# Optimization experiments

Hardware: AMD Instinct MI355X
Metric: run time of the kernel (lower is better)

The kernel has to match this reference:

```python
import jax, jax.numpy as jnp
import numpy as np

NUM_HEADS = 4
KEY_DIMS = 32  # c // num_heads


def rel_to_abs(x):
    # x: [B, N, W, 2W-1] relative logits -> [B, N, W, W] absolute logits
    b, n, w, _ = x.shape
    x = jnp.pad(x, ((0, 0), (0, 0), (0, 0), (0, 1)))           # [b,n,w,2w]
    x = x.reshape(b, n, w * 2 * w)
    x = jnp.pad(x, ((0, 0), (0, 0), (0, w - 1)))
    x = x.reshape(b, n, w + 1, 2 * w - 1)
    return x[:, :, :w, w - 1:]


def rel_logits_1d(q, rel_k):
    # q: [B, heads, X, Y, d], rel_k: [2Y-1, d] -> [B, heads, X, X, Y, Y]
    b, nh, xx, yy, d = q.shape
    rl = jnp.einsum('bhxyd,md->bhxym', q, rel_k)               # [b,h,x,y,2y-1]
    rl = rel_to_abs(rl.reshape(b, nh * xx, yy, 2 * yy - 1))    # [b,h*x,y,y]
    rl = rl.reshape(b, nh, xx, 1, yy, yy)
    return jnp.broadcast_to(rl, (b, nh, xx, xx, yy, yy))


def relative_position_bias(pos_q, pos_emb_h, pos_emb_w):
    # pos_q: [B, heads, H, W, d] -> bias [B, heads, H, W, H, W]
    rw = rel_logits_1d(pos_q, pos_emb_w)                        # [b,h,H,H,W,W]
    rw = rw.transpose(0, 1, 2, 4, 3, 5)                         # [b,h,H,W,H,W]
    rh = rel_logits_1d(pos_q.transpose(0, 1, 3, 2, 4), pos_emb_h)  # [b,h,W,W,H,H]
    rh = rh.transpose(0, 1, 4, 2, 5, 3)                         # [b,h,H,W,H,W]
    return rw + rh


def setup_inputs() -> dict:
    key = jax.random.key(0)
    k1, k2, k3, k4 = jax.random.split(key, 4)
    B, H, W, C = 2, 64, 64, 128
    qk_dims = NUM_HEADS * KEY_DIMS  # 128
    out_channels = C
    x = jax.random.normal(k1, (B, H, W, C), dtype=jnp.float32)
    w_qkv = jax.random.normal(k2, (C, 2 * qk_dims + out_channels), dtype=jnp.float32) * 0.05
    pos_emb_h = jax.random.normal(k3, (2 * H - 1, KEY_DIMS), dtype=jnp.float32) * 0.05
    pos_emb_w = jax.random.normal(k4, (2 * W - 1, KEY_DIMS), dtype=jnp.float32) * 0.05
    return {'x': x, 'w_qkv': w_qkv, 'pos_emb_h': pos_emb_h, 'pos_emb_w': pos_emb_w}


def reference(x, w_qkv, pos_emb_h, pos_emb_w):
    B, H, W, C = x.shape
    nh, kd = NUM_HEADS, KEY_DIMS
    qk_dims = nh * kd
    oc = C
    scale = 1.0 / float(kd) ** 0.5

    qkv = jnp.einsum('bhwc,cd->bhwd', x, w_qkv)                 # 1x1 conv, no bias
    q, k, v = jnp.split(qkv, [qk_dims, 2 * qk_dims], axis=-1)
    L = H * W
    q = q.reshape(B, L, nh, kd).transpose(0, 2, 1, 3)           # [B,nh,L,kd]
    k = k.reshape(B, L, nh, kd).transpose(0, 2, 1, 3)           # [B,nh,L,kd]
    v = v.reshape(B, L, nh, oc // nh).transpose(0, 2, 1, 3)     # [B,nh,L,dv]

    pos_q = q.reshape(B, nh, H, W, kd)
    pos = relative_position_bias(pos_q, pos_emb_h, pos_emb_w).reshape(B, nh, L, L)

    scores = jnp.einsum('bnqd,bnkd->bnqk', q, k) * scale + pos  # [B,nh,L,L]
    attn = jax.nn.softmax(scores, axis=-1)
    out = jnp.einsum('bnqk,bnkd->bnqd', attn, v)                # [B,nh,L,dv]
    out = out.transpose(0, 2, 1, 3).reshape(B, H, W, oc)
    return out
```

## Files before the change

### kernel.cpp

```cpp
#include <hip/hip_runtime.h>
#include <hip/hip_bf16.h>
#include <math.h>

#define B_  2
#define NH  4
#define HH  64
#define WW  64
#define KD  32
#define L_  4096
#define BN_ 8
#define LOG2E 1.4426950408889634f
#define KSCALE (0.17677669529663687f * 1.4426950408889634f)
#define FIXED_M 10.0f

typedef float    f32x4  __attribute__((ext_vector_type(4), may_alias));
typedef _Float16 half8  __attribute__((ext_vector_type(8), may_alias));
typedef _Float16 half4  __attribute__((ext_vector_type(4), may_alias));
typedef __fp16   fp16x2 __attribute__((ext_vector_type(2)));
typedef unsigned uint4v __attribute__((ext_vector_type(4)));

__device__ __forceinline__ float fexp2(float x) {
#if __has_builtin(__builtin_amdgcn_exp2f)
    return __builtin_amdgcn_exp2f(x);
#else
    return __expf(x * 0.69314718056f);
#endif
}

__device__ __forceinline__ unsigned pack2u(float a, float b) {
    fp16x2 t = __builtin_amdgcn_cvt_pkrtz(a, b);
    union { fp16x2 i; unsigned o; } u;
    u.i = t;
    return u.o;
}

__global__ __launch_bounds__(256) void qkv_gemm(const float* __restrict__ x,
                                                const float* __restrict__ w,
                                                _Float16* __restrict__ q_h,
                                                _Float16* __restrict__ k_h,
                                                _Float16* __restrict__ vt_h) {
    __shared__ __align__(16) char smem[34816];
    _Float16* xs  = (_Float16*)smem;
    _Float16* wsT = (_Float16*)(smem + 17408);

    const int mt = blockIdx.x % 128;
    const int nt = blockIdx.x / 128;
    const int m0 = mt * 64, n0 = nt * 64;
    const int tid = threadIdx.x;
    const int wv = tid >> 6, lane = tid & 63;
    const int l16 = lane & 15, quad = lane >> 4;

    #pragma unroll
    for (int i = 0; i < 8; i++) {
        const int idx = i * 256 + tid;
        const int row = idx >> 5, c4 = (idx & 31) * 4;
        const float4 v = *(const float4*)&x[(size_t)(m0 + row) * 128 + c4];
        half4 h;
        h[0] = (_Float16)v.x; h[1] = (_Float16)v.y;
        h[2] = (_Float16)v.z; h[3] = (_Float16)v.w;
        *(half4*)&xs[row * 136 + c4] = h;
    }
    #pragma unroll
    for (int i = 0; i < 8; i++) {
        const int idx = i * 256 + tid;
        const int k = idx >> 4, c4 = (idx & 15) * 4;
        const float4 v = *(const float4*)&w[(size_t)k * 384 + n0 + c4];
        wsT[(c4 + 0) * 136 + k] = (_Float16)v.x;
        wsT[(c4 + 1) * 136 + k] = (_Float16)v.y;
        wsT[(c4 + 2) * 136 + k] = (_Float16)v.z;
        wsT[(c4 + 3) * 136 + k] = (_Float16)v.w;
    }
    __syncthreads();

    f32x4 acc[4] = {{0.f,0.f,0.f,0.f},{0.f,0.f,0.f,0.f},
                    {0.f,0.f,0.f,0.f},{0.f,0.f,0.f,0.f}};
    half8 af[4];
    #pragma unroll
    for (int kc = 0; kc < 4; kc++)
        af[kc] = *(const half8*)&xs[(wv * 16 + l16) * 136 + kc * 32 + quad * 8];
    #pragma unroll
    for (int ns = 0; ns < 4; ns++)
        #pragma unroll
        for (int kc = 0; kc < 4; kc++) {
            const half8 bf = *(const half8*)&wsT[(ns * 16 + l16) * 136 + kc * 32 + quad * 8];
            acc[ns] = __builtin_amdgcn_mfma_f32_16x16x32_f16(af[kc], bf, acc[ns], 0, 0, 0);
        }

    const int which = n0 >> 7;
    const int nc = n0 & 127;
    const int b = m0 >> 12;
    if (which < 2) {
        _Float16* dst = (which == 0) ? q_h : k_h;
        const float mult = (which == 1) ? KSCALE : 1.0f;
        #pragma unroll
        for (int ns = 0; ns < 4; ns++) {
            const int col = nc + ns * 16 + l16;
            const int bn = b * NH + (col >> 5);
            const int d = col & 31;
            #pragma unroll
            for (int r = 0; r < 4; r++) {
                const int l = (m0 & 4095) + wv * 16 + quad * 4 + r;
                dst[((size_t)bn * L_ + l) * 32 + d] = (_Float16)(acc[ns][r] * mult);
            }
        }
    } else {
        __syncthreads();
        float* img = (float*)smem;
        #pragma unroll
        for (int ns = 0; ns < 4; ns++) {
            const int chan = ns * 16 + l16;
            const int h = chan >> 5, d = chan & 31;
            #pragma unroll
            for (int r = 0; r < 4; r++) {
                const int p = wv * 16 + quad * 4 + r;
                const int y = p >> 5, p32 = p & 31;
                const int q4 = (p32 >> 2) & 3;
                const int j = ((p32 >> 4) & 1) * 4 + (p32 & 3);
                const int fidx = h * 2048 + (y * 2 + (d >> 4)) * 512
                               + (q4 * 16 + (d & 15)) * 8 + j;
                img[fidx + (fidx >> 4)] = acc[ns][r];
            }
        }
        __syncthreads();
        const int ktg = (m0 & 4095) >> 6;
        #pragma unroll
        for (int h = 0; h < 2; h++) {
            const int head = (nc >> 5) + h;
            const int bn = b * NH + head;
            const int fbase = h * 2048 + tid * 8;
            const int sbase = fbase + (fbase >> 4);
            half8 o;
            #pragma unroll
            for (int e = 0; e < 8; e++) o[e] = (_Float16)img[sbase + e];
            *(half8*)(vt_h + (size_t)bn * 131072 + ktg * 2048 + tid * 8) = o;
        }
    }
}

__global__ __launch_bounds__(512, 4) void attn_mfma(
    const _Float16* __restrict__ q_h,
    const _Float16* __restrict__ k_h,
    const _Float16* __restrict__ vt_h,
    const float* __restrict__ emb_h,
    const float* __restrict__ emb_w,
    float* __restrict__ out)
{
    __shared__ __align__(16) char smem[33792];

    const int bi   = blockIdx.x;
    const int bn   = bi & 7;
    const int w1   = bi >> 3;
    const int tid  = threadIdx.x;
    const int wv   = tid >> 6;
    const int qwv  = wv & 3;
    const int kh   = wv >> 2;
    const int lane = tid & 63;
    const int l16  = lane & 15;
    const int quad = lane >> 4;
    const int q0   = qwv * 16;

    float* Rl = (float*)smem;

    const half8 aq = *(const half8*)(q_h +
        (((size_t)bn * L_ + (q0 + l16) * 64 + w1) * 32 + quad * 8));

    const _Float16* Kbase = k_h  + (size_t)bn * L_ * 32;
    const _Float16* Vtile = vt_h + (size_t)bn * 131072;
    const int lo = lane * 8;
    const int kt0 = kh * 32;
    const int phase = wv & 3;

    int kt = kt0 + phase;
    half8 kf[4];
    #pragma unroll
    for (int sub = 0; sub < 4; sub++)
        kf[sub] = *(const half8*)(Kbase + (size_t)(kt * 64 + sub * 16 + l16) * 32 + quad * 8);

    f32x4 qwT[4];
    #pragma unroll
    for (int sub = 0; sub < 4; sub++) {
        const float* ew = emb_w + (size_t)(sub * 16 + l16 - w1 + 63) * 32 + quad * 8;
        const float4 e0 = *(const float4*)ew;
        const float4 e1 = *(const float4*)(ew + 4);
        union { uint4v u; half8 h; } ua;
        ua.u[0] = pack2u(e0.x * LOG2E, e0.y * LOG2E);
        ua.u[1] = pack2u(e0.z * LOG2E, e0.w * LOG2E);
        ua.u[2] = pack2u(e1.x * LOG2E, e1.y * LOG2E);
        ua.u[3] = pack2u(e1.z * LOG2E, e1.w * LOG2E);
        f32x4 z = {-FIXED_M, -FIXED_M, -FIXED_M, -FIXED_M};
        qwT[sub] = __builtin_amdgcn_mfma_f32_16x16x32_f16(ua.h, aq, z, 0, 0, 0);
    }

    #pragma unroll
    for (int ji = 0; ji < 4; ji++) {
        const int jt = kh * 4 + ji;
        const int j = min(jt * 16 + l16, 126);
        const float* eh = emb_h + (size_t)j * 32 + quad * 8;
        const float4 e0 = *(const float4*)eh;
        const float4 e1 = *(const float4*)(eh + 4);
        union { uint4v u; half8 h; } ub;
        ub.u[0] = pack2u(e0.x * LOG2E, e0.y * LOG2E);
        ub.u[1] = pack2u(e0.z * LOG2E, e0.w * LOG2E);
        ub.u[2] = pack2u(e1.x * LOG2E, e1.y * LOG2E);
        ub.u[3] = pack2u(e1.z * LOG2E, e1.w * LOG2E);
        f32x4 z = {0.f, 0.f, 0.f, 0.f};
        const f32x4 C = __builtin_amdgcn_mfma_f32_16x16x32_f16(aq, ub.h, z, 0, 0, 0);
        #pragma unroll
        for (int r = 0; r < 4; r++)
            Rl[(q0 + quad * 4 + r) * 132 + jt * 16 + l16] = C[r];
    }
    __syncthreads();

    f32x4 O0 = {0.f, 0.f, 0.f, 0.f}, O1 = {0.f, 0.f, 0.f, 0.f};
    float l0 = 0.f, l1 = 0.f;
    const float* qh_ptr = Rl + (q0 + l16) * 132 + 63 - (q0 + l16);
    float qh_cur = qh_ptr[kt];
#if __has_builtin(__builtin_amdgcn_fdot2)
    fp16x2 onep;
    { union { unsigned u; fp16x2 h; } uo; uo.u = pack2u(1.0f, 1.0f); onep = uo.h; }
#endif

    #pragma unroll 4
    for (int i = 0; i < 32; i++) {
        const _Float16* tb = Vtile + kt * 2048;
        const half8 va00 = *(const half8*)(tb + lo);
        const half8 va10 = *(const half8*)(tb + 512 + lo);
        const half8 va01 = *(const half8*)(tb + 1024 + lo);
        const half8 va11 = *(const half8*)(tb + 1536 + lo);

        const f32x4 S0 = __builtin_amdgcn_mfma_f32_16x16x32_f16(kf[0], aq, qwT[0], 0, 0, 0);
        const f32x4 S1 = __builtin_amdgcn_mfma_f32_16x16x32_f16(kf[1], aq, qwT[1], 0, 0, 0);
        const f32x4 S2 = __builtin_amdgcn_mfma_f32_16x16x32_f16(kf[2], aq, qwT[2], 0, 0, 0);
        const f32x4 S3 = __builtin_amdgcn_mfma_f32_16x16x32_f16(kf[3], aq, qwT[3], 0, 0, 0);

        const int ktn = kt0 + (((kt - kt0) + 1) & 31);
        #pragma unroll
        for (int sub = 0; sub < 4; sub++)
            kf[sub] = *(const half8*)(Kbase + (size_t)(ktn * 64 + sub * 16 + l16) * 32 + quad * 8);
        const float qh_next = qh_ptr[ktn];

        union { uint4v u; half8 h; } pb0, pb1;
        const float a0 = fexp2(S0[0] + qh_cur), a1 = fexp2(S0[1] + qh_cur);
        const float a2 = fexp2(S0[2] + qh_cur), a3 = fexp2(S0[3] + qh_cur);
        const float a4 = fexp2(S1[0] + qh_cur), a5 = fexp2(S1[1] + qh_cur);
        const float a6 = fexp2(S1[2] + qh_cur), a7 = fexp2(S1[3] + qh_cur);
        pb0.u[0] = pack2u(a0, a1); pb0.u[1] = pack2u(a2, a3);
        pb0.u[2] = pack2u(a4, a5); pb0.u[3] = pack2u(a6, a7);
        const float b0 = fexp2(S2[0] + qh_cur), b1 = fexp2(S2[1] + qh_cur);
        const float b2 = fexp2(S2[2] + qh_cur), b3 = fexp2(S2[3] + qh_cur);
        const float b4 = fexp2(S3[0] + qh_cur), b5 = fexp2(S3[1] + qh_cur);
        const float b6 = fexp2(S3[2] + qh_cur), b7 = fexp2(S3[3] + qh_cur);
        pb1.u[0] = pack2u(b0, b1); pb1.u[1] = pack2u(b2, b3);
        pb1.u[2] = pack2u(b4, b5); pb1.u[3] = pack2u(b6, b7);

        O0 = __builtin_amdgcn_mfma_f32_16x16x32_f16(va00, pb0.h, O0, 0, 0, 0);
        O0 = __builtin_amdgcn_mfma_f32_16x16x32_f16(va01, pb1.h, O0, 0, 0, 0);
        O1 = __builtin_amdgcn_mfma_f32_16x16x32_f16(va10, pb0.h, O1, 0, 0, 0);
        O1 = __builtin_amdgcn_mfma_f32_16x16x32_f16(va11, pb1.h, O1, 0, 0, 0);

#if __has_builtin(__builtin_amdgcn_fdot2)
        {
            union { unsigned u; fp16x2 h; } c0, c1, c2, c3;
            c0.u = pb0.u[0]; c1.u = pb0.u[1]; c2.u = pb0.u[2]; c3.u = pb0.u[3];
            l0 = __builtin_amdgcn_fdot2(c0.h, onep, l0, false);
            l0 = __builtin_amdgcn_fdot2(c1.h, onep, l0, false);
            l0 = __builtin_amdgcn_fdot2(c2.h, onep, l0, false);
            l0 = __builtin_amdgcn_fdot2(c3.h, onep, l0, false);
            c0.u = pb1.u[0]; c1.u = pb1.u[1]; c2.u = pb1.u[2]; c3.u = pb1.u[3];
            l1 = __builtin_amdgcn_fdot2(c0.h, onep, l1, false);
            l1 = __builtin_amdgcn_fdot2(c1.h, onep, l1, false);
            l1 = __builtin_amdgcn_fdot2(c2.h, onep, l1, false);
            l1 = __builtin_amdgcn_fdot2(c3.h, onep, l1, false);
        }
#else
        l0 += ((a0 + a1) + (a2 + a3)) + ((a4 + a5) + (a6 + a7));
        l1 += ((b0 + b1) + (b2 + b3)) + ((b4 + b5) + (b6 + b7));
#endif

        qh_cur = qh_next;
        kt = ktn;
    }

    float l = l0 + l1;
    l += __shfl_xor(l, 16);
    l += __shfl_xor(l, 32);

    __syncthreads();
    float (*mO)[32][17] = (float(*)[32][17])smem;
    float* mL = (float*)(smem + 17408);
    #pragma unroll
    for (int r = 0; r < 4; r++) {
        mO[wv][quad * 4 + r][l16]      = O0[r];
        mO[wv][16 + quad * 4 + r][l16] = O1[r];
    }
    if (quad == 0) mL[wv * 16 + l16] = l;
    __syncthreads();

    const int q  = tid >> 3;
    const int dg = tid & 7;
    const int qg = q >> 4, ql = q & 15;
    const float denom = mL[qg * 16 + ql] + mL[(qg + 4) * 16 + ql];
    const float inv = 1.0f / denom;
    float4 o;
    o.x = (mO[qg][dg * 4 + 0][ql] + mO[qg + 4][dg * 4 + 0][ql]) * inv;
    o.y = (mO[qg][dg * 4 + 1][ql] + mO[qg + 4][dg * 4 + 1][ql]) * inv;
    o.z = (mO[qg][dg * 4 + 2][ql] + mO[qg + 4][dg * 4 + 2][ql]) * inv;
    o.w = (mO[qg][dg * 4 + 3][ql] + mO[qg + 4][dg * 4 + 3][ql]) * inv;
    const int head = bn & 3, bb = bn >> 2;
    *(float4*)&out[(((size_t)bb * 64 + q) * 64 + w1) * 128 + head * 32 + dg * 4] = o;
}

extern "C" void kernel_launch(void* const* d_in, const int* in_sizes, int n_in,
                              void* d_out, int out_size, void* d_ws, size_t ws_size,
                              hipStream_t stream) {
    const float* x     = (const float*)d_in[0];
    const float* w_qkv = (const float*)d_in[1];
    const float* emb_h = (const float*)d_in[2];
    const float* emb_w = (const float*)d_in[3];
    float* out = (float*)d_out;

    _Float16* q_h  = (_Float16*)d_ws;
    _Float16* k_h  = q_h + (size_t)BN_ * L_ * KD;
    _Float16* vt_h = k_h + (size_t)BN_ * L_ * KD;

    qkv_gemm<<<768, 256, 0, stream>>>(x, w_qkv, q_h, k_h, vt_h);
    attn_mfma<<<512, 512, 0, stream>>>(q_h, k_h, vt_h, emb_h, emb_w, out);
}
```

Baseline: 121.2 us.

## Process two query columns per block with 1024-thread attention blocks

The attention kernel now launches 256 blocks of 1024 threads, and each block handles two adjacent w1 columns instead of one. Each wave gets a private relative-logit scratch region, and the final reduction is remapped across the two columns. This halves the block count, which may improve sharing of the K/V tiles through cache and lower per-block setup cost. The price is double the LDS per block and 1024-thread blocks, which can reduce occupancy; the key-tile phase staggering also drops from four phases to two.

```diff
diff --git a/kernel.cpp b/kernel.cpp
--- a/kernel.cpp
+++ b/kernel.cpp
@@ -137,7 +137,7 @@
     }
 }
 
-__global__ __launch_bounds__(512, 4) void attn_mfma(
+__global__ __launch_bounds__(1024, 4) void attn_mfma(
     const _Float16* __restrict__ q_h,
     const _Float16* __restrict__ k_h,
     const _Float16* __restrict__ vt_h,
@@ -145,21 +145,24 @@
     const float* __restrict__ emb_w,
     float* __restrict__ out)
 {
-    __shared__ __align__(16) char smem[33792];
-
-    const int bi   = blockIdx.x;
-    const int bn   = bi & 7;
-    const int w1   = bi >> 3;
-    const int tid  = threadIdx.x;
-    const int wv   = tid >> 6;
-    const int qwv  = wv & 3;
-    const int kh   = wv >> 2;
-    const int lane = tid & 63;
-    const int l16  = lane & 15;
-    const int quad = lane >> 4;
-    const int q0   = qwv * 16;
-
-    float* Rl = (float*)smem;
+    __shared__ __align__(16) char smem[67584];
+
+    const int bi    = blockIdx.x;
+    const int bn    = bi & 7;
+    const int wpair = bi >> 3;
+    const int tid   = threadIdx.x;
+    const int wv    = tid >> 6;
+    const int kh    = wv >> 3;
+    const int ws    = wv & 7;
+    const int qg    = ws >> 1;
+    const int wo    = ws & 1;
+    const int w1    = wpair * 2 + wo;
+    const int lane  = tid & 63;
+    const int l16   = lane & 15;
+    const int quad  = lane >> 4;
+    const int q0    = qg * 16;
+
+    float* Rw = (float*)smem + ws * 2112;
 
     const half8 aq = *(const half8*)(q_h +
         (((size_t)bn * L_ + (q0 + l16) * 64 + w1) * 32 + quad * 8));
@@ -168,7 +171,7 @@
     const _Float16* Vtile = vt_h + (size_t)bn * 131072;
     const int lo = lane * 8;
     const int kt0 = kh * 32;
-    const int phase = wv & 3;
+    const int phase = ws & 1;
 
     int kt = kt0 + phase;
     half8 kf[4];
@@ -207,13 +210,13 @@
         const f32x4 C = __builtin_amdgcn_mfma_f32_16x16x32_f16(aq, ub.h, z, 0, 0, 0);
         #pragma unroll
         for (int r = 0; r < 4; r++)
-            Rl[(q0 + quad * 4 + r) * 132 + jt * 16 + l16] = C[r];
+            Rw[(quad * 4 + r) * 132 + jt * 16 + l16] = C[r];
     }
     __syncthreads();
 
     f32x4 O0 = {0.f, 0.f, 0.f, 0.f}, O1 = {0.f, 0.f, 0.f, 0.f};
     float l0 = 0.f, l1 = 0.f;
-    const float* qh_ptr = Rl + (q0 + l16) * 132 + 63 - (q0 + l16);
+    const float* qh_ptr = Rw + l16 * 132 + 63 - (q0 + l16);
     float qh_cur = qh_ptr[kt];
 #if __has_builtin(__builtin_amdgcn_fdot2)
     fp16x2 onep;
@@ -287,7 +290,7 @@
 
     __syncthreads();
     float (*mO)[32][17] = (float(*)[32][17])smem;
-    float* mL = (float*)(smem + 17408);
+    float* mL = (float*)(smem + 34816);
     #pragma unroll
     for (int r = 0; r < 4; r++) {
         mO[wv][quad * 4 + r][l16]      = O0[r];
@@ -296,18 +299,23 @@
     if (quad == 0) mL[wv * 16 + l16] = l;
     __syncthreads();
 
-    const int q  = tid >> 3;
-    const int dg = tid & 7;
-    const int qg = q >> 4, ql = q & 15;
-    const float denom = mL[qg * 16 + ql] + mL[(qg + 4) * 16 + ql];
+    const int wo_o = tid >> 9;
+    const int rest = tid & 511;
+    const int h1   = rest >> 3;
+    const int dg   = rest & 7;
+    const int qgo  = h1 >> 4, ql = h1 & 15;
+    const int wsA  = qgo * 2 + wo_o;
+    const int wsB  = wsA + 8;
+    const float denom = mL[wsA * 16 + ql] + mL[wsB * 16 + ql];
     const float inv = 1.0f / denom;
     float4 o;
-    o.x = (mO[qg][dg * 4 + 0][ql] + mO[qg + 4][dg * 4 + 0][ql]) * inv;
-    o.y = (mO[qg][dg * 4 + 1][ql] + mO[qg + 4][dg * 4 + 1][ql]) * inv;
-    o.z = (mO[qg][dg * 4 + 2][ql] + mO[qg + 4][dg * 4 + 2][ql]) * inv;
-    o.w = (mO[qg][dg * 4 + 3][ql] + mO[qg + 4][dg * 4 + 3][ql]) * inv;
+    o.x = (mO[wsA][dg * 4 + 0][ql] + mO[wsB][dg * 4 + 0][ql]) * inv;
+    o.y = (mO[wsA][dg * 4 + 1][ql] + mO[wsB][dg * 4 + 1][ql]) * inv;
+    o.z = (mO[wsA][dg * 4 + 2][ql] + mO[wsB][dg * 4 + 2][ql]) * inv;
+    o.w = (mO[wsA][dg * 4 + 3][ql] + mO[wsB][dg * 4 + 3][ql]) * inv;
     const int head = bn & 3, bb = bn >> 2;
-    *(float4*)&out[(((size_t)bb * 64 + q) * 64 + w1) * 128 + head * 32 + dg * 4] = o;
+    const int w1o = wpair * 2 + wo_o;
+    *(float4*)&out[(((size_t)bb * 64 + h1) * 64 + w1o) * 128 + head * 32 + dg * 4] = o;
 }
 
 extern "C" void kernel_launch(void* const* d_in, const int* in_sizes, int n_in,
@@ -324,5 +332,5 @@
     _Float16* vt_h = k_h + (size_t)BN_ * L_ * KD;
 
     qkv_gemm<<<768, 256, 0, stream>>>(x, w_qkv, q_h, k_h, vt_h);
-    attn_mfma<<<512, 512, 0, stream>>>(q_h, k_h, vt_h, emb_h, emb_w, out);
-}
+    attn_mfma<<<256, 1024, 0, stream>>>(q_h, k_h, vt_h, emb_h, emb_w, out);
+}
```

New measurement: 123.7 us. +2.0%, slower.
